# Optimization experiments

Hardware: AMD Instinct MI355X
Metric: run time of the kernel (lower is better)

## Reference

```python
import jax, jax.numpy as jnp
import numpy as np

THETA = 10.0      # spike threshold
TAU_SR = 10.0     # synaptic (psp) alpha-kernel time constant
TAU_REF = 1.0     # refractory alpha-kernel time constant
SCALE_REF = 2.0   # refractory kernel scale (refKernel = -2*theta*alpha)
TS = 1.0          # simulation step


def psp(x):
    """SLAYER psp: causal conv along time with alpha kernel k[n] = (n*Ts/tau)*exp(1 - n*Ts/tau),
    realized exactly as a 2-state linear IIR recurrence. x: (..., T)."""
    a = jnp.float32(np.exp(-TS / TAU_SR))
    c = jnp.float32(np.e * TS / TAU_SR)
    xt = jnp.moveaxis(x, -1, 0)  # (T, ...)
    z = jnp.zeros_like(xt[0])

    def step(carry, xin):
        p, q = carry
        q = a * q + a * p          # q[n] = sum_m x[m]*(n-m)*a^(n-m)
        p = a * p + xin            # p[n] = sum_m x[m]*a^(n-m)
        return (p, q), c * q       # k-convolution output (k[0] = 0)

    _, y = jax.lax.scan(step, (z, z), xt)
    return jnp.moveaxis(y, 0, -1)


def spike(x):
    """SLAYER spike: threshold with refractory feedback. At each step the membrane is
    psp input plus -2*theta * (alpha-kernel conv of past spikes); spike amplitude 1/Ts = 1.
    Refractory alpha kernel realized with the same 2-state IIR. x: (..., T)."""
    a = jnp.float32(np.exp(-TS / TAU_REF))
    c = jnp.float32(np.e * TS / TAU_REF)
    xt = jnp.moveaxis(x, -1, 0)
    z = jnp.zeros_like(xt[0])

    def step(carry, ut):
        p, q = carry
        q = a * q + a * p
        u = ut - SCALE_REF * THETA * c * q   # membrane = input psp + refractory response
        s = (u >= THETA).astype(ut.dtype)
        p = a * p + s                        # spike feeds refractory state (k[0]=0 so no self-effect)
        return (p, q), s

    _, y = jax.lax.scan(step, (z, z), xt)
    return jnp.moveaxis(y, 0, -1)


def conv_t(x, w, pad):
    """Per-timestep 2D conv: x (B,Cin,H,W,T), w (Cout,Cin,k,k); time folded into batch."""
    b, cin, h, wd, t = x.shape
    xt = jnp.moveaxis(x, -1, 1).reshape(b * t, cin, h, wd)
    y = jax.lax.conv_general_dilated(xt, w, (1, 1), [(pad, pad), (pad, pad)])
    y = y.reshape(b, t, y.shape[1], y.shape[2], y.shape[3])
    return jnp.moveaxis(y, 1, -1)


def pool2(x):
    """SLAYER pool: zero-pad odd dims, 2x2 sum with constant weight 1.1*theta, stride 2."""
    b, ch, h, wd, t = x.shape
    ph, pw = (-h) % 2, (-wd) % 2
    x = jnp.pad(x, ((0, 0), (0, 0), (0, ph), (0, pw), (0, 0)))
    h2, w2 = (h + ph) // 2, (wd + pw) // 2
    x = x.reshape(b, ch, h2, 2, w2, 2, t).sum(axis=(3, 5))
    return 1.1 * THETA * x


def setup_inputs() -> dict:
    key = jax.random.key(0)
    ks = jax.random.split(key, 6)
    B, T = 4, 300
    s_in = (jax.random.uniform(ks[0], (B, 2, 34, 34, T)) < 0.03).astype(jnp.float32)
    def w(k, shape, scale):
        fan_in = int(np.prod(shape[1:]))
        return jax.random.normal(k, shape, jnp.float32) * (scale / np.sqrt(fan_in))
    return {
        "s_in": s_in,
        "Wc1": w(ks[1], (24, 2, 5, 5), 10.0),    # weightScale=10
        "Wc2": w(ks[2], (48, 24, 3, 3), 15.0),   # weightScale=15
        "Wc3": w(ks[3], (96, 48, 3, 3), 15.0),   # weightScale=15
        "Wd4a": w(ks[4], (256, 96, 5, 5), 1.0),
        "Wd4b": w(ks[5], (10, 256), 1.0),
    }


def reference(s_in, Wc1, Wc2, Wc3, Wd4a, Wd4b):
    x = spike(psp(conv_t(s_in, Wc1, 2)))                  # (B,24,34,34,T)
    x = spike(psp(pool2(x)))                              # (B,24,17,17,T)
    x = spike(psp(conv_t(x, Wc2, 1)))                     # (B,48,17,17,T)
    x = spike(psp(pool2(x)))                              # (B,48,9,9,T)
    x = spike(psp(conv_t(x, Wc3, 1)))                     # (B,96,9,9,T)
    x = spike(psp(pool2(x)))                              # (B,96,5,5,T)
    x = spike(psp(jnp.einsum('bchwt,ochw->bot', x, Wd4a)))  # (B,256,T)
    x = spike(psp(jnp.einsum('bnt,on->bot', x, Wd4b)))      # (B,10,T)
    return x
```

## Files before the change

kernel.cpp:

```cpp
#include <hip/hip_runtime.h>


#define TT 300

#define A1 0.9048374180359595f
#define C1 0.2718281828459045f
#define A2 0.36787944117144233f
#define C2 2.718281828459045f
#define KREF (20.0f * C2)
#define THETA_F 10.0f

typedef float v2f __attribute__((ext_vector_type(2)));
typedef float f32x4 __attribute__((ext_vector_type(4)));
typedef short bf16x8 __attribute__((ext_vector_type(8)));

struct IIR {
  float p1, q1, p2, q2;
  __device__ IIR() : p1(0.f), q1(0.f), p2(0.f), q2(0.f) {}
  __device__ inline float step(float xin) {
    q1 = A1 * q1 + A1 * p1;
    float y = C1 * q1;
    p1 = A1 * p1 + xin;
    q2 = A2 * q2 + A2 * p2;
    float u = y - KREF * q2;
    float s = (u >= THETA_F) ? 1.0f : 0.0f;
    p2 = A2 * p2 + s;
    return s;
  }
};

__global__ __launch_bounds__(256) void transpose_rc(const float* __restrict__ in,
                                                    float* __restrict__ out,
                                                    int R, int C) {
  __shared__ float tile[64][65];
  int c0 = blockIdx.x * 64, r0 = blockIdx.y * 64;
  int tx = threadIdx.x & 63, ty = threadIdx.x >> 6;
  for (int i = ty; i < 64; i += 4) {
    int r = r0 + i, c = c0 + tx;
    if (r < R && c < C) tile[i][tx] = in[(long)r * C + c];
  }
  __syncthreads();
  for (int i = ty; i < 64; i += 4) {
    int c = c0 + i, r = r0 + tx;
    if (c < C && r < R) out[(long)c * R + r] = tile[tx][i];
  }
}

__device__ inline unsigned rne_bf16_bits(float f) {
  unsigned u = __float_as_uint(f);
  return (u + 0x7FFFu + ((u >> 16) & 1u)) >> 16;
}
template <int CIN, int KS, int CO, int MT, int KC>
__global__ __launch_bounds__(256) void prep_mfma(const float* __restrict__ Wc,
                                                 ushort* __restrict__ Wm) {
  constexpr int K = CIN * KS * KS;
  constexpr int PLANE = MT * KC * 512;
  int i = blockIdx.x * 256 + threadIdx.x;
  if (i >= PLANE) return;
  int e = i & 7, l = (i >> 3) & 63;
  int rest = i >> 9;
  int kc = rest % KC, m = rest / KC;
  int co = m * 16 + (l & 15);
  int k = kc * 32 + (l >> 4) * 8 + e;
  float w = 0.f;
  if (k < K && co < CO) {
    int ci = k / (KS * KS), r = k % (KS * KS), dy = r / KS, dx = r % KS;
    w = Wc[((co * CIN + ci) * KS + dy) * KS + dx];
  }
  unsigned b0 = rne_bf16_bits(w);
  float f0 = __uint_as_float(b0 << 16);
  float d1 = w - f0;
  unsigned b1 = rne_bf16_bits(d1);
  float f1 = __uint_as_float(b1 << 16);
  unsigned b2 = rne_bf16_bits(d1 - f1);
  Wm[i] = (ushort)b0;
  Wm[PLANE + i] = (ushort)b1;
  Wm[2 * PLANE + i] = (ushort)b2;
}

template <int CIN, int HW, int KS, int PAD, int CO, int RS, int NW, int NSUB>
__global__ __launch_bounds__(NW * 64) void conv_mfma_d(const float* __restrict__ S,
                                                       const ushort* __restrict__ Wm,
                                                       float* __restrict__ U) {
  constexpr int PH = HW + 2 * PAD;
  constexpr int K = CIN * KS * KS;
  constexpr int KC = (K + 31) / 32;
  constexpr int MT = (CO + 15) / 16;
  constexpr int N = HW * HW;
  constexpr int NT = (N + 15) / 16;
  constexpr int NG = (NT + NSUB - 1) / NSUB;
  constexpr int TILE = CIN * PH * RS;
  constexpr int KPAD = KC * 32;
  __shared__ float lin[TILE];
  __shared__ int koff[KPAD];
  const int t = blockIdx.x, b = blockIdx.y, B = gridDim.y;
  const int tid = threadIdx.x;

  for (int i = tid; i < TILE; i += NW * 64) lin[i] = 0.f;
  for (int k = tid; k < KPAD; k += NW * 64) {
    int ci = k / (KS * KS), r = k % (KS * KS), dy = r / KS, dx = r % KS;
    koff[k] = (k < K) ? (ci * PH * RS + dy * RS + dx) : 0;
  }
  __syncthreads();
  const float* src = S + ((long)t * B + b) * (CIN * N);
  for (int i = tid; i < CIN * N; i += NW * 64) {
    int ci = i / N, r = i % N, iy = r / HW, ix = r % HW;
    lin[ci * PH * RS + (iy + PAD) * RS + ix + PAD] = src[i];
  }
  __syncthreads();

  const int lane = tid & 63;
  const int wv = tid >> 6;
  const int g = lane >> 4;
  const int col = lane & 15;

  bf16x8 af[3 * MT * KC];
#pragma unroll
  for (int f = 0; f < 3 * MT * KC; ++f)
    af[f] = *(const bf16x8*)(Wm + (long)f * 512 + lane * 8);

  for (int grp = wv; grp < NG; grp += NW) {
    const int px0 = grp * (16 * NSUB);
    bool vs[NSUB];
    int pxb[NSUB];
    bf16x8 bf[NSUB][KC];
#pragma unroll
    for (int s = 0; s < NSUB; ++s) {
      int px = px0 + s * 16 + col;
      vs[s] = px < N;
      int ppx = vs[s] ? px : 0;
      int y = ppx / HW, x = ppx % HW;
      pxb[s] = y * RS + x;
#pragma unroll
      for (int kc = 0; kc < KC; ++kc) {
        bf16x8 v;
#pragma unroll
        for (int e = 0; e < 8; ++e) {
          float val = lin[pxb[s] + koff[kc * 32 + g * 8 + e]];
          v[e] = (short)(__float_as_uint(val) >> 16);
        }
        bf[s][kc] = v;
      }
    }

#pragma unroll
    for (int m = 0; m < MT; ++m) {
      f32x4 acc[NSUB];
#pragma unroll
      for (int s = 0; s < NSUB; ++s) acc[s] = (f32x4){0.f, 0.f, 0.f, 0.f};
#pragma unroll
      for (int p = 0; p < 3; ++p) {
#pragma unroll
        for (int kc = 0; kc < KC; ++kc) {
          bf16x8 a = af[(p * MT + m) * KC + kc];
#pragma unroll
          for (int s = 0; s < NSUB; ++s)
            acc[s] = __builtin_amdgcn_mfma_f32_16x16x32_bf16(a, bf[s][kc], acc[s], 0, 0, 0);
        }
      }
      const int co0 = m * 16 + g * 4;
#pragma unroll
      for (int s = 0; s < NSUB; ++s) {
        if (vs[s]) {
          float* up = U + (((long)t * B + b) * CO + co0) * N + px0 + s * 16 + col;
#pragma unroll
          for (int j = 0; j < 4; ++j)
            if (co0 + j < CO) up[(long)j * N] = acc[s][j];
        }
      }
    }
  }
}

template <int CIN, int HW, int KS, int PAD, int CO, int RS, int NW, int MCHUNK>
__global__ __launch_bounds__(NW * 64) void conv_mfma_c(const float* __restrict__ S,
                                                       const ushort* __restrict__ Wm,
                                                       float* __restrict__ U) {
  constexpr int PH = HW + 2 * PAD;
  constexpr int K = CIN * KS * KS;
  constexpr int KC = (K + 31) / 32;
  constexpr int MT = (CO + 15) / 16;
  constexpr int N = HW * HW;
  constexpr int NT = (N + 15) / 16;
  constexpr int TILE = CIN * PH * RS;
  constexpr int KPAD = KC * 32;
  constexpr int NCH = MT / MCHUNK;
  constexpr int CROWS = MCHUNK * 16;
  __shared__ float lin[TILE];
  __shared__ int koff[KPAD];
  __shared__ float cst[CROWS * N];
  const int t = blockIdx.x, b = blockIdx.y, B = gridDim.y;
  const int tid = threadIdx.x;

  for (int i = tid; i < TILE; i += NW * 64) lin[i] = 0.f;
  for (int k = tid; k < KPAD; k += NW * 64) {
    int ci = k / (KS * KS), r = k % (KS * KS), dy = r / KS, dx = r % KS;
    koff[k] = (k < K) ? (ci * PH * RS + dy * RS + dx) : 0;
  }
  __syncthreads();
  const float* src = S + ((long)t * B + b) * (CIN * N);
  for (int i = tid; i < CIN * N; i += NW * 64) {
    int ci = i / N, r = i % N, iy = r / HW, ix = r % HW;
    lin[ci * PH * RS + (iy + PAD) * RS + ix + PAD] = src[i];
  }
  __syncthreads();

  const int lane = tid & 63;
  const int wv = tid >> 6;
  const int g = lane >> 4;
  const int col = lane & 15;

  for (int ch = 0; ch < NCH; ++ch) {
    for (int nt = wv; nt < NT; nt += NW) {
      int px = nt * 16 + col;
      bool vpx = px < N;
      int ppx = vpx ? px : 0;
      int y = ppx / HW, x = ppx % HW;
      const int pxbase = y * RS + x;

      bf16x8 bf[KC];
#pragma unroll
      for (int kc = 0; kc < KC; ++kc) {
        bf16x8 v;
#pragma unroll
        for (int e = 0; e < 8; ++e) {
          float val = lin[pxbase + koff[kc * 32 + g * 8 + e]];
          v[e] = (short)(__float_as_uint(val) >> 16);
        }
        bf[kc] = v;
      }

#pragma unroll
      for (int ml = 0; ml < MCHUNK; ++ml) {
        const int m = ch * MCHUNK + ml;
        f32x4 acc = {0.f, 0.f, 0.f, 0.f};
#pragma unroll
        for (int p = 0; p < 3; ++p) {
#pragma unroll
          for (int kc = 0; kc < KC; ++kc) {
            bf16x8 a = *(const bf16x8*)(Wm + ((long)(p * MT + m) * KC + kc) * 512 + lane * 8);
            acc = __builtin_amdgcn_mfma_f32_16x16x32_bf16(a, bf[kc], acc, 0, 0, 0);
          }
        }
        if (vpx) {
          const int r0 = ml * 16 + g * 4;
#pragma unroll
          for (int j = 0; j < 4; ++j) cst[(r0 + j) * N + px] = acc[j];
        }
      }
    }
    __syncthreads();
    const f32x4* cs = (const f32x4*)cst;
    f32x4* ug = (f32x4*)(U + (((long)t * B + b) * CO + ch * CROWS) * N);
    for (int i = tid; i < CROWS * N / 4; i += NW * 64) ug[i] = cs[i];
    __syncthreads();
  }
}

template <int C, int HIN, int HOUT>
__global__ __launch_bounds__(128) void ppp4_tm(const float* __restrict__ U,
                                               float* __restrict__ out, int B) {
  const int NOUT = B * C * HOUT * HOUT;
  const long SIN = (long)B * C * HIN * HIN;
  int id = blockIdx.x * 128 + threadIdx.x;
  int sub = id & 3, m = id >> 2;
  bool active = m < NOUT;
  int mm = active ? m : 0;
  int x2 = mm % HOUT;
  int y2 = (mm / HOUT) % HOUT;
  int c = (mm / (HOUT * HOUT)) % C;
  int b = mm / (C * HOUT * HOUT);
  int iy = 2 * y2 + (sub >> 1), ix = 2 * x2 + (sub & 1);
  bool valid = active && iy < HIN && ix < HIN;
  const float* base = U + ((long)(b * C + c) * HIN + iy) * HIN + ix;
  bool writer = active && (sub == 0);
  float* op = out + mm;
  IIR si, so;
  float pr0 = valid ? base[0] : 0.f;
  float pr1 = valid ? base[SIN] : 0.f;
  float pr2 = valid ? base[2 * SIN] : 0.f;
  float pr3 = valid ? base[3 * SIN] : 0.f;
  for (int tb = 0; tb < TT; tb += 4) {
    float a0 = pr0, a1 = pr1, a2 = pr2, a3 = pr3;
    const float* nb = base + (long)(tb + 4) * SIN;
    pr0 = valid ? nb[0] : 0.f;
    pr1 = valid ? nb[SIN] : 0.f;
    pr2 = valid ? nb[2 * SIN] : 0.f;
    pr3 = valid ? nb[3 * SIN] : 0.f;
    {
      float s = si.step(a0);
      float v = s + __shfl_xor(s, 1); v += __shfl_xor(v, 2);
      float o = so.step(11.0f * v);
      if (writer) op[(long)tb * NOUT] = o;
    }
    {
      float s = si.step(a1);
      float v = s + __shfl_xor(s, 1); v += __shfl_xor(v, 2);
      float o = so.step(11.0f * v);
      if (writer) op[(long)(tb + 1) * NOUT] = o;
    }
    {
      float s = si.step(a2);
      float v = s + __shfl_xor(s, 1); v += __shfl_xor(v, 2);
      float o = so.step(11.0f * v);
      if (writer) op[(long)(tb + 2) * NOUT] = o;
    }
    {
      float s = si.step(a3);
      float v = s + __shfl_xor(s, 1); v += __shfl_xor(v, 2);
      float o = so.step(11.0f * v);
      if (writer) op[(long)(tb + 3) * NOUT] = o;
    }
  }
}

__global__ __launch_bounds__(256) void dense7k(const float* __restrict__ S,
                                               const float* __restrict__ Wt,
                                               float* __restrict__ P) {
  const int r0 = blockIdx.x * 16 + (threadIdx.x >> 6) * 4;
  const int kz = blockIdx.y;
  const int lane = threadIdx.x & 63;
  const float* s0 = S + (long)r0 * 2400;
  const float* s1 = s0 + 2400;
  const float* s2 = s0 + 4800;
  const float* s3 = s0 + 7200;
  const float* wp = Wt + lane * 4;
  v2f aA[4], aB[4];
#pragma unroll
  for (int o = 0; o < 4; ++o) { aA[o] = (v2f)(0.f); aB[o] = (v2f)(0.f); }
  const int k0 = kz * 300, k1 = k0 + 300;
  for (int k = k0; k < k1; k += 4) {
    float4 a0 = *(const float4*)(s0 + k);
    float4 a1 = *(const float4*)(s1 + k);
    float4 a2 = *(const float4*)(s2 + k);
    float4 a3 = *(const float4*)(s3 + k);
#define DSTEP(KK, AX)                                                        \
    {                                                                        \
      float4 w = *(const float4*)(wp + (long)(k + KK) * 256);                \
      v2f pA, pB;                                                            \
      pA.x = a0.AX; pA.y = a1.AX; pB.x = a2.AX; pB.y = a3.AX;                \
      aA[0] += pA * w.x; aA[1] += pA * w.y; aA[2] += pA * w.z; aA[3] += pA * w.w; \
      aB[0] += pB * w.x; aB[1] += pB * w.y; aB[2] += pB * w.z; aB[3] += pB * w.w; \
    }
    DSTEP(0, x) DSTEP(1, y) DSTEP(2, z) DSTEP(3, w)
#undef DSTEP
  }
  float* p = P + (long)kz * 307200 + (long)r0 * 256 + lane * 4;
#pragma unroll
  for (int o = 0; o < 4; ++o) p[o] = aA[o].x;
#pragma unroll
  for (int o = 0; o < 4; ++o) p[256 + o] = aA[o].y;
#pragma unroll
  for (int o = 0; o < 4; ++o) p[512 + o] = aB[o].x;
#pragma unroll
  for (int o = 0; o < 4; ++o) p[768 + o] = aB[o].y;
}

__global__ __launch_bounds__(256) void reduce8(const float* __restrict__ P,
                                               float* __restrict__ U7) {
  int i = blockIdx.x * 256 + threadIdx.x;
  if (i >= 76800) return;
  const float4* p = (const float4*)P;
  float4 a = p[i];
#pragma unroll
  for (int kz = 1; kz < 8; ++kz) {
    float4 b = p[(long)kz * 76800 + i];
    a.x += b.x; a.y += b.y; a.z += b.z; a.w += b.w;
  }
  ((float4*)U7)[i] = a;
}

__global__ __launch_bounds__(128) void psp7(const float* __restrict__ U7,
                                            float* __restrict__ out) {
  int n = blockIdx.x * 128 + threadIdx.x;
  IIR st;
  float pr0 = U7[n], pr1 = U7[1024 + n], pr2 = U7[2048 + n], pr3 = U7[3072 + n];
  for (int tb = 0; tb < TT; tb += 4) {
    float a0 = pr0, a1 = pr1, a2 = pr2, a3 = pr3;
    const float* nb = U7 + (long)(tb + 4) * 1024 + n;
    pr0 = nb[0]; pr1 = nb[1024]; pr2 = nb[2048]; pr3 = nb[3072];
    out[(long)tb * 1024 + n] = st.step(a0);
    out[(long)(tb + 1) * 1024 + n] = st.step(a1);
    out[(long)(tb + 2) * 1024 + n] = st.step(a2);
    out[(long)(tb + 3) * 1024 + n] = st.step(a3);
  }
}

__global__ __launch_bounds__(256) void dense8(const float* __restrict__ S,
                                              const float* __restrict__ W,
                                              float* __restrict__ U) {
  int id = blockIdx.x * 256 + threadIdx.x;
  if (id >= 12000) return;
  int o = id % 10, row = id / 10;
  const float* sr = S + (long)row * 256;
  const float* wr = W + o * 256;
  float acc = 0.f;
  for (int k = 0; k < 256; k += 4) {
    float4 a = *(const float4*)(sr + k);
    float4 w = *(const float4*)(wr + k);
    acc += a.x * w.x; acc += a.y * w.y; acc += a.z * w.z; acc += a.w * w.w;
  }
  U[id] = acc;
}

__global__ void psp8_out(const float* __restrict__ U, float* __restrict__ out) {
  int n = threadIdx.x;
  bool act = n < 40;
  int nn = act ? n : 0;
  IIR st;
  float pr0 = U[nn], pr1 = U[40 + nn], pr2 = U[80 + nn], pr3 = U[120 + nn];
  for (int tb = 0; tb < TT; tb += 4) {
    float a0 = pr0, a1 = pr1, a2 = pr2, a3 = pr3;
    const float* nb = U + (long)(tb + 4) * 40 + nn;
    pr0 = nb[0]; pr1 = nb[40]; pr2 = nb[80]; pr3 = nb[120];
    float o0 = st.step(a0), o1 = st.step(a1), o2 = st.step(a2), o3 = st.step(a3);
    if (act) {
      out[nn * TT + tb] = o0;
      out[nn * TT + tb + 1] = o1;
      out[nn * TT + tb + 2] = o2;
      out[nn * TT + tb + 3] = o3;
    }
  }
}

extern "C" void kernel_launch(void* const* d_in, const int* in_sizes, int n_in,
                              void* d_out, int out_size, void* d_ws, size_t ws_size,
                              hipStream_t stream) {
  const float* s_in = (const float*)d_in[0];
  const float* Wc1  = (const float*)d_in[1];
  const float* Wc2  = (const float*)d_in[2];
  const float* Wc3  = (const float*)d_in[3];
  const float* Wd4a = (const float*)d_in[4];
  const float* Wd4b = (const float*)d_in[5];

  float* Buf1 = (float*)d_ws;
  float* Buf2 = Buf1 + 33292800;
  float* s2   = Buf2;
  float* s4   = Buf2 + 8323200;
  float* Wt4a = Buf2 + 12988800;
  float* T0   = Buf2 + 13910400;
  float* s7   = Buf2 + 16737840;
  float* P7   = Buf2 + 17045040;
  float* U7   = Buf2 + 19502640;
  float* s6   = Buf2;
  float* U8   = Buf1;
  ushort* Wm1 = (ushort*)P7;
  ushort* Wm2 = Wm1 + 18432;
  ushort* Wm3 = Wm1 + 50688;

  transpose_rc<<<dim3(5, 145), 256, 0, stream>>>(s_in, T0, 9248, 300);
  transpose_rc<<<dim3(38, 4), 256, 0, stream>>>(Wd4a, Wt4a, 256, 2400);
  prep_mfma<2, 5, 24, 2, 2><<<24, 256, 0, stream>>>(Wc1, Wm1);
  prep_mfma<24, 3, 48, 3, 7><<<42, 256, 0, stream>>>(Wc2, Wm2);
  prep_mfma<48, 3, 96, 6, 14><<<168, 256, 0, stream>>>(Wc3, Wm3);

  conv_mfma_d<2, 34, 5, 2, 24, 39, 8, 4><<<dim3(300, 4), 512, 0, stream>>>(T0, Wm1, Buf1);
  ppp4_tm<24, 34, 17><<<867, 128, 0, stream>>>(Buf1, s2, 4);
  conv_mfma_c<24, 17, 3, 1, 48, 19, 8, 1><<<dim3(300, 4), 512, 0, stream>>>(s2, Wm2, Buf1);
  ppp4_tm<48, 17, 9><<<486, 128, 0, stream>>>(Buf1, s4, 4);
  conv_mfma_c<48, 9, 3, 1, 96, 13, 6, 6><<<dim3(300, 4), 384, 0, stream>>>(s4, Wm3, Buf1);
  ppp4_tm<96, 9, 5><<<300, 128, 0, stream>>>(Buf1, s6, 4);
  dense7k<<<dim3(75, 8), 256, 0, stream>>>(s6, Wt4a, P7);
  reduce8<<<300, 256, 0, stream>>>(P7, U7);
  psp7<<<8, 128, 0, stream>>>(U7, s7);
  dense8<<<47, 256, 0, stream>>>(s7, Wd4b, U8);
  psp8_out<<<1, 64, 0, stream>>>(U8, (float*)d_out);
}
```

Baseline: 592.7 us.

## Repartition conv MFMA work by output-channel tile per wave, drop LDS staging

The conv2/conv3 kernels now give each wave a fixed 16-row output-channel tile and a contiguous range of pixel tiles. Each wave keeps its weight fragments in registers for the whole range and writes results straight to global memory, so the shared-memory staging buffer and its extra barriers are gone. The trade-off is that B fragments are regathered from LDS once per pixel tile and p pass, which raises LDS reads, and register pressure grows with per-wave accumulator arrays. Launch configurations change to 6 waves for both layers.

```diff
diff --git a/kernel.cpp b/kernel.cpp
--- a/kernel.cpp
+++ b/kernel.cpp
@@ -172,23 +172,21 @@
   }
 }
 
-template <int CIN, int HW, int KS, int PAD, int CO, int RS, int NW, int MCHUNK>
-__global__ __launch_bounds__(NW * 64) void conv_mfma_c(const float* __restrict__ S,
+template <int CIN, int HW, int KS, int PAD, int CO, int RS, int NW, int WPM>
+__global__ __launch_bounds__(NW * 64) void conv_mfma_m(const float* __restrict__ S,
                                                        const ushort* __restrict__ Wm,
                                                        float* __restrict__ U) {
   constexpr int PH = HW + 2 * PAD;
   constexpr int K = CIN * KS * KS;
   constexpr int KC = (K + 31) / 32;
-  constexpr int MT = (CO + 15) / 16;
+  constexpr int MT = CO / 16;
   constexpr int N = HW * HW;
   constexpr int NT = (N + 15) / 16;
+  constexpr int CH = (NT + WPM - 1) / WPM;
   constexpr int TILE = CIN * PH * RS;
   constexpr int KPAD = KC * 32;
-  constexpr int NCH = MT / MCHUNK;
-  constexpr int CROWS = MCHUNK * 16;
   __shared__ float lin[TILE];
   __shared__ int koff[KPAD];
-  __shared__ float cst[CROWS * N];
   const int t = blockIdx.x, b = blockIdx.y, B = gridDim.y;
   const int tid = threadIdx.x;
 
@@ -209,51 +207,52 @@
   const int wv = tid >> 6;
   const int g = lane >> 4;
   const int col = lane & 15;
-
-  for (int ch = 0; ch < NCH; ++ch) {
-    for (int nt = wv; nt < NT; nt += NW) {
-      int px = nt * 16 + col;
-      bool vpx = px < N;
-      int ppx = vpx ? px : 0;
-      int y = ppx / HW, x = ppx % HW;
-      const int pxbase = y * RS + x;
-
-      bf16x8 bf[KC];
+  const int m = wv / WPM;
+  const int nt0 = (wv % WPM) * CH;
+
+  bool vpx[CH];
+  int pxb[CH];
+#pragma unroll
+  for (int i = 0; i < CH; ++i) {
+    int px = (nt0 + i) * 16 + col;
+    vpx[i] = px < N;
+    int ppx = vpx[i] ? px : 0;
+    int y = ppx / HW, x = ppx % HW;
+    pxb[i] = y * RS + x;
+  }
+
+  f32x4 acc[CH];
+#pragma unroll
+  for (int i = 0; i < CH; ++i) acc[i] = (f32x4){0.f, 0.f, 0.f, 0.f};
+
+  for (int p = 0; p < 3; ++p) {
+    bf16x8 af[KC];
+#pragma unroll
+    for (int kc = 0; kc < KC; ++kc)
+      af[kc] = *(const bf16x8*)(Wm + ((long)(p * MT + m) * KC + kc) * 512 + lane * 8);
+#pragma unroll
+    for (int i = 0; i < CH; ++i) {
 #pragma unroll
       for (int kc = 0; kc < KC; ++kc) {
         bf16x8 v;
 #pragma unroll
         for (int e = 0; e < 8; ++e) {
-          float val = lin[pxbase + koff[kc * 32 + g * 8 + e]];
+          float val = lin[pxb[i] + koff[kc * 32 + g * 8 + e]];
           v[e] = (short)(__float_as_uint(val) >> 16);
         }
-        bf[kc] = v;
+        acc[i] = __builtin_amdgcn_mfma_f32_16x16x32_bf16(af[kc], v, acc[i], 0, 0, 0);
       }
-
-#pragma unroll
-      for (int ml = 0; ml < MCHUNK; ++ml) {
-        const int m = ch * MCHUNK + ml;
-        f32x4 acc = {0.f, 0.f, 0.f, 0.f};
-#pragma unroll
-        for (int p = 0; p < 3; ++p) {
-#pragma unroll
-          for (int kc = 0; kc < KC; ++kc) {
-            bf16x8 a = *(const bf16x8*)(Wm + ((long)(p * MT + m) * KC + kc) * 512 + lane * 8);
-            acc = __builtin_amdgcn_mfma_f32_16x16x32_bf16(a, bf[kc], acc, 0, 0, 0);
-          }
-        }
-        if (vpx) {
-          const int r0 = ml * 16 + g * 4;
-#pragma unroll
-          for (int j = 0; j < 4; ++j) cst[(r0 + j) * N + px] = acc[j];
-        }
-      }
-    }
-    __syncthreads();
-    const f32x4* cs = (const f32x4*)cst;
-    f32x4* ug = (f32x4*)(U + (((long)t * B + b) * CO + ch * CROWS) * N);
-    for (int i = tid; i < CROWS * N / 4; i += NW * 64) ug[i] = cs[i];
-    __syncthreads();
+    }
+  }
+
+  const int co0 = m * 16 + g * 4;
+  float* ub = U + (((long)t * B + b) * CO + co0) * N;
+#pragma unroll
+  for (int j = 0; j < 4; ++j) {
+#pragma unroll
+    for (int i = 0; i < CH; ++i) {
+      if (vpx[i]) ub[(long)j * N + (nt0 + i) * 16 + col] = acc[i][j];
+    }
   }
 }
 
@@ -456,9 +455,9 @@
 
   conv_mfma_d<2, 34, 5, 2, 24, 39, 8, 4><<<dim3(300, 4), 512, 0, stream>>>(T0, Wm1, Buf1);
   ppp4_tm<24, 34, 17><<<867, 128, 0, stream>>>(Buf1, s2, 4);
-  conv_mfma_c<24, 17, 3, 1, 48, 19, 8, 1><<<dim3(300, 4), 512, 0, stream>>>(s2, Wm2, Buf1);
+  conv_mfma_m<24, 17, 3, 1, 48, 19, 6, 2><<<dim3(300, 4), 384, 0, stream>>>(s2, Wm2, Buf1);
   ppp4_tm<48, 17, 9><<<486, 128, 0, stream>>>(Buf1, s4, 4);
-  conv_mfma_c<48, 9, 3, 1, 96, 13, 6, 6><<<dim3(300, 4), 384, 0, stream>>>(s4, Wm3, Buf1);
+  conv_mfma_m<48, 9, 3, 1, 96, 13, 6, 1><<<dim3(300, 4), 384, 0, stream>>>(s4, Wm3, Buf1);
   ppp4_tm<96, 9, 5><<<300, 128, 0, stream>>>(Buf1, s6, 4);
   dense7k<<<dim3(75, 8), 256, 0, stream>>>(s6, Wt4a, P7);
   reduce8<<<300, 256, 0, stream>>>(P7, U7);
```

New measurement: 835.2 us. 40.9% more time.
